# Optimization experiments

Measured on AMD Instinct MI355X. Metric: run time of the kernel, lower is better.

## Reference

```python
import jax, jax.numpy as jnp
import numpy as np
from math import sqrt

MIN_WINDOW, MAX_WINDOW = 1.0, 10000.0


def rope_consecutive(x):
    # x: [B, S, H, D]; TE 'consecutive' rotary: pairs are adjacent (even, odd) lanes.
    d = x.shape[-1]
    half = d // 2
    fraction = 2.0 * jnp.arange(half, dtype=jnp.float32) / d
    time_scales = MIN_WINDOW * (MAX_WINDOW / MIN_WINDOW) ** fraction          # [D/2]
    time_scales = jnp.repeat(time_scales, 2)                                   # [D]
    positions = jnp.arange(x.shape[1], dtype=jnp.float32)                      # [S]
    sinusoid = positions[None, :, None, None] / time_scales                    # [1,S,1,D]
    sin, cos = jnp.sin(sinusoid), jnp.cos(sinusoid)
    idx = jnp.arange(d)
    odd = (idx % 2) == 1                                                       # [D]
    # even lanes take left neighbor (roll -1), odd lanes take right neighbor (roll +1)
    x_shifted = jnp.where(odd, jnp.roll(x, 1, axis=-1), jnp.roll(x, -1, axis=-1))
    sign = jnp.where(odd, 1.0, -1.0)
    return (x * cos + x_shifted * sin * sign).astype(x.dtype)


def setup_inputs() -> dict:
    key = jax.random.key(0)
    k1, k2, k3 = jax.random.split(key, 3)
    B, S, M, H, D = 4, 2048, 2048, 16, 128
    x = jax.random.normal(k1, (B, S, M), dtype=jnp.float32)
    Wqkv = jax.random.normal(k2, (M, 3, H, D), dtype=jnp.float32) / sqrt(M)
    Wo = jax.random.normal(k3, (H * D, M), dtype=jnp.float32) / sqrt(H * D)
    return {"x": x, "Wqkv": Wqkv, "Wo": Wo}


def reference(x, Wqkv, Wo):
    # x: [B,S,M]; Wqkv: [M,3,H,D]; Wo: [H*D,M]
    B, S, M = x.shape
    H, D = Wqkv.shape[2], Wqkv.shape[3]
    qkv = jnp.einsum('bsm,mthd->bsthd', x, Wqkv)  # packed BS3HD projection
    q, k, v = qkv[:, :, 0], qkv[:, :, 1], qkv[:, :, 2]  # each [B,S,H,D]
    q = rope_consecutive(q)
    k = rope_consecutive(k)
    scale = 1.0 / sqrt(D)
    scores = jnp.einsum('bqhd,bkhd->bhqk', q, k) * scale  # [B,H,S,S]
    causal = jnp.tril(jnp.ones((S, S), dtype=bool))
    scores = jnp.where(causal[None, None], scores, jnp.finfo(scores.dtype).min)
    probs = jax.nn.softmax(scores, axis=-1)
    ctx = jnp.einsum('bhqk,bkhd->bqhd', probs, v)  # [B,S,H,D]
    out = jnp.einsum('bqhd,xm->bqm', ctx, jnp.zeros((0, 0))) if False else ctx.reshape(B, S, H * D) @ Wo
    return out
```

## Files before the change

kernel.cpp:

```cpp
#include <hip/hip_runtime.h>
#include <hip/hip_bf16.h>

#define B_ 4
#define S_ 2048
#define M_ 2048
#define H_ 16
#define D_ 128
#define ROWS (B_*S_)
#define CQKV (3*H_*D_)

typedef __bf16 bf16x8 __attribute__((ext_vector_type(8)));
typedef float f32x4 __attribute__((ext_vector_type(4)));
typedef unsigned short u16x8 __attribute__((ext_vector_type(8)));
typedef unsigned short u16x4 __attribute__((ext_vector_type(4)));

__device__ __forceinline__ unsigned short f2bf(float x) {
    unsigned u = __builtin_bit_cast(unsigned, x);
    u += 0x7fffu + ((u >> 16) & 1u);
    return (unsigned short)(u >> 16);
}
__device__ __forceinline__ float bf2f(unsigned short u) {
    return __builtin_bit_cast(float, (unsigned)u << 16);
}

__device__ __forceinline__ void gld_lds16(const unsigned short* g, unsigned short* l) {
    __builtin_amdgcn_global_load_lds(
        (__attribute__((address_space(1))) void*)g,
        (__attribute__((address_space(3))) void*)l,
        16, 0, 0);
}


__global__ __launch_bounds__(256) void cvt_bf16(const float* __restrict__ in,
                                                unsigned short* __restrict__ out) {
    int idx = (blockIdx.x * 256 + threadIdx.x) * 4;
    float4 v = *(const float4*)&in[idx];
    u16x4 o = { f2bf(v.x), f2bf(v.y), f2bf(v.z), f2bf(v.w) };
    *(u16x4*)&out[idx] = o;
}

__global__ __launch_bounds__(256) void cvt_transpose(const float* __restrict__ in,
                                                     unsigned short* __restrict__ out,
                                                     int R, int C) {
    __shared__ unsigned short tile[32][33];
    int c0 = blockIdx.x * 32, r0 = blockIdx.y * 32;
    int tx = threadIdx.x, ty = threadIdx.y;
#pragma unroll
    for (int i = 0; i < 4; ++i)
        tile[ty + i * 8][tx] = f2bf(in[(size_t)(r0 + ty + i * 8) * C + c0 + tx]);
    __syncthreads();
#pragma unroll
    for (int i = 0; i < 4; ++i)
        out[(size_t)(c0 + ty + i * 8) * R + r0 + tx] = tile[tx][ty + i * 8];
}

__global__ __launch_bounds__(256) void vtrans(const unsigned short* __restrict__ in,
                                              unsigned short* __restrict__ out) {
    __shared__ unsigned short tile[32][33];
    int bh = blockIdx.z;
    int d0 = blockIdx.x * 32, s0 = blockIdx.y * 32;
    const unsigned short* ib = in + (size_t)bh * S_ * D_;
    unsigned short* ob = out + (size_t)bh * S_ * D_;
    int tx = threadIdx.x, ty = threadIdx.y;
#pragma unroll
    for (int i = 0; i < 4; ++i)
        tile[ty + i * 8][tx] = ib[(size_t)(s0 + ty + i * 8) * D_ + d0 + tx];
    __syncthreads();
#pragma unroll
    for (int i = 0; i < 4; ++i)
        ob[(size_t)(d0 + ty + i * 8) * S_ + s0 + tx] = tile[tx][ty + i * 8];
}


#define BM2 256
#define BN2 256
#define BK2 64
#define NT2 (M_/BK2)

#define STAGE(p_, u_, mat_, h_) do {                                                     \
        const unsigned short* _s = (mat_) ? Bg : Ag;                                     \
        const size_t _r = (size_t)((((mat_) ? c0 : r0) + (h_) * 128) + w * 8 + srow) * M_ \
                          + (u_) * BK2 + scol;                                           \
        unsigned short* _l = &lds[(p_) * 32768 + (mat_) * 16384 + (h_) * 8192 + w * 512]; \
        gld_lds16(&_s[_r], _l);                                                          \
        gld_lds16(&_s[_r + (size_t)64 * M_], _l + 4096);                                 \
    } while (0)

#define BAR() asm volatile("s_barrier" ::: "memory")

#define GEMM_MAIN_LOOP()                                                                  \
    const int srow = lane >> 3;                                                           \
    const int scol = ((lane & 7) ^ srow) * 8;                                             \
    const int axor = lcol & 7;                                                            \
    const int k0off = (lq ^ axor) * 8;                                                    \
    const int k1off = ((4 | lq) ^ axor) * 8;                                              \
    const int arow = wr * 8192 + lcol * 64;                                               \
    const int brow = 16384 + (wc >> 1) * 8192 + ((wc & 1) * 64 + lcol) * 64;              \
    f32x4 acc[8][4];                                                                      \
    _Pragma("unroll") for (int i = 0; i < 8; ++i)                                         \
        _Pragma("unroll") for (int j = 0; j < 4; ++j) acc[i][j] = (f32x4){0.f,0.f,0.f,0.f};\
    STAGE(0, 0, 0, 0); STAGE(0, 0, 0, 1); STAGE(0, 0, 1, 0); STAGE(0, 0, 1, 1);           \
    STAGE(1, 1, 1, 0); STAGE(1, 1, 1, 1);                                                 \
    asm volatile("s_waitcnt vmcnt(4)" ::: "memory");                                      \
    BAR();                                                                                \
    bf16x8 a[4][2], b[4][2];                                                              \
    for (int t = 0; t < NT2; ++t) {                                                       \
        const int bo = (t & 1) * 32768;                                                   \
        const int pn = (t + 1) & 1;                                                       \
        const int u1 = (t + 1 < NT2) ? (t + 1) : (NT2 - 1);                               \
        const int u2 = (t + 2 < NT2) ? (t + 2) : (NT2 - 1);                               \
        _Pragma("unroll") for (int i = 0; i < 4; ++i) {                                   \
            a[i][0] = *(const bf16x8*)&lds[bo + arow + i * 1024 + k0off];                  \
            a[i][1] = *(const bf16x8*)&lds[bo + arow + i * 1024 + k1off];                  \
        }                                                                                 \
        _Pragma("unroll") for (int j = 0; j < 2; ++j) {                                   \
            b[j][0] = *(const bf16x8*)&lds[bo + brow + j * 1024 + k0off];                  \
            b[j][1] = *(const bf16x8*)&lds[bo + brow + j * 1024 + k1off];                  \
        }                                                                                 \
        STAGE(pn, u1, 0, 0);                                                              \
        BAR();                                                                            \
        __builtin_amdgcn_s_setprio(1);                                                    \
        _Pragma("unroll") for (int i = 0; i < 4; ++i)                                     \
            _Pragma("unroll") for (int j = 0; j < 2; ++j) {                               \
                acc[i][j] = __builtin_amdgcn_mfma_f32_16x16x32_bf16(a[i][0], b[j][0], acc[i][j], 0, 0, 0); \
                acc[i][j] = __builtin_amdgcn_mfma_f32_16x16x32_bf16(a[i][1], b[j][1], acc[i][j], 0, 0, 0); \
            }                                                                             \
        __builtin_amdgcn_s_setprio(0);                                                    \
        BAR();                                                                            \
        _Pragma("unroll") for (int j = 2; j < 4; ++j) {                                   \
            b[j][0] = *(const bf16x8*)&lds[bo + brow + j * 1024 + k0off];                  \
            b[j][1] = *(const bf16x8*)&lds[bo + brow + j * 1024 + k1off];                  \
        }                                                                                 \
        STAGE(pn, u1, 0, 1);                                                              \
        BAR();                                                                            \
        __builtin_amdgcn_s_setprio(1);                                                    \
        _Pragma("unroll") for (int i = 0; i < 4; ++i)                                     \
            _Pragma("unroll") for (int j = 2; j < 4; ++j) {                               \
                acc[i][j] = __builtin_amdgcn_mfma_f32_16x16x32_bf16(a[i][0], b[j][0], acc[i][j], 0, 0, 0); \
                acc[i][j] = __builtin_amdgcn_mfma_f32_16x16x32_bf16(a[i][1], b[j][1], acc[i][j], 0, 0, 0); \
            }                                                                             \
        __builtin_amdgcn_s_setprio(0);                                                    \
        BAR();                                                                            \
        _Pragma("unroll") for (int i = 0; i < 4; ++i) {                                   \
            a[i][0] = *(const bf16x8*)&lds[bo + arow + (i + 4) * 1024 + k0off];            \
            a[i][1] = *(const bf16x8*)&lds[bo + arow + (i + 4) * 1024 + k1off];            \
        }                                                                                 \
        STAGE(t & 1, u2, 1, 0);                                                           \
        BAR();                                                                            \
        __builtin_amdgcn_s_setprio(1);                                                    \
        _Pragma("unroll") for (int i = 0; i < 4; ++i)                                     \
            _Pragma("unroll") for (int j = 2; j < 4; ++j) {                               \
                acc[i + 4][j] = __builtin_amdgcn_mfma_f32_16x16x32_bf16(a[i][0], b[j][0], acc[i + 4][j], 0, 0, 0); \
                acc[i + 4][j] = __builtin_amdgcn_mfma_f32_16x16x32_bf16(a[i][1], b[j][1], acc[i + 4][j], 0, 0, 0); \
            }                                                                             \
        __builtin_amdgcn_s_setprio(0);                                                    \
        BAR();                                                                            \
        STAGE(t & 1, u2, 1, 1);                                                           \
        BAR();                                                                            \
        __builtin_amdgcn_s_setprio(1);                                                    \
        _Pragma("unroll") for (int i = 0; i < 4; ++i)                                     \
            _Pragma("unroll") for (int j = 0; j < 2; ++j) {                               \
                acc[i + 4][j] = __builtin_amdgcn_mfma_f32_16x16x32_bf16(a[i][0], b[j][0], acc[i + 4][j], 0, 0, 0); \
                acc[i + 4][j] = __builtin_amdgcn_mfma_f32_16x16x32_bf16(a[i][1], b[j][1], acc[i + 4][j], 0, 0, 0); \
            }                                                                             \
        __builtin_amdgcn_s_setprio(0);                                                    \
        asm volatile("s_waitcnt vmcnt(4)" ::: "memory");                                  \
        BAR();                                                                            \
    }


__global__ __launch_bounds__(512, 2) void gemm_qkv_rope(
    const unsigned short* __restrict__ xb,
    const unsigned short* __restrict__ wT,
    unsigned short* __restrict__ qg,
    unsigned short* __restrict__ kg,
    unsigned short* __restrict__ vg) {
    __shared__ unsigned short lds[65536];

    const int tid = threadIdx.x;
    const int lane = tid & 63;
    const int w = tid >> 6;
    const int wr = w >> 2;
    const int wc = w & 3;
    const int lcol = lane & 15;
    const int lq = lane >> 4;

    const int lin = (int)(blockIdx.y * gridDim.x + blockIdx.x);
    const int swz = (lin & 7) * 96 + (lin >> 3);
    const int r0 = (swz / 24) * BM2;
    const int c0 = (swz % 24) * BN2;

    const unsigned short* Ag = xb;
    const unsigned short* Bg = wT;

    GEMM_MAIN_LOOP()

    asm volatile("s_waitcnt vmcnt(0)" ::: "memory");
    __syncthreads();

    const int tix = c0 >> 11;
    const bool do_rope = (tix < 2);
#pragma unroll
    for (int j = 0; j < 4; ++j) {
        const int lcolT = wc * 64 + j * 16 + lcol;
        const int d = lcolT & 127;
        float inv_ts = 0.f, sw = 0.f, cw = 1.f;
        if (do_rope) {
            inv_ts = exp2f(-(float)(d >> 1) * (13.28771237954945f / 64.0f));
            __sincosf(inv_ts, &sw, &cw);
        }
#pragma unroll
        for (int i = 0; i < 8; ++i) {
            const int rbase = wr * 128 + i * 16 + lq * 4;
            float sn = 0.f, cs = 1.f;
            if (do_rope) {
                int s0 = (r0 + rbase) & 2047;
                __sincosf((float)s0 * inv_ts, &sn, &cs);
            }
#pragma unroll
            for (int r = 0; r < 4; ++r) {
                const int rowT = rbase + r;
                float val = acc[i][j][r];
                float pr = __shfl_xor(val, 1);
                float v2 = val;
                if (do_rope) {
                    v2 = (d & 1) ? (val * cs + pr * sn) : (val * cs - pr * sn);
                    float ns = sn * cw + cs * sw;
                    float nc = cs * cw - sn * sw;
                    sn = ns; cs = nc;
                }
                const int ch = lcolT >> 3;
                const int cph = (ch & ~7) | ((ch ^ rowT) & 7);
                lds[rowT * 256 + cph * 8 + (lcolT & 7)] = f2bf(v2);
            }
        }
    }
    __syncthreads();

    const int hh = (c0 & 2047) >> 7;
    unsigned short* dst = (tix == 0) ? qg : (tix == 1) ? kg : vg;
    const int li = tid & 15;
    const int g = tid >> 4;
#pragma unroll
    for (int gi = 0; gi < 16; ++gi) {
        const int rh = g + gi * 32;
        const int row = rh >> 1, half = rh & 1;
        const int clog = half * 16 + li;
        const int cph = (clog & ~7) | ((clog ^ row) & 7);
        u16x8 v = *(const u16x8*)&lds[row * 256 + cph * 8];
        const int gr = r0 + row;
        const int s = gr & 2047, bb = gr >> 11;
        *(u16x8*)&dst[(size_t)((bb * H_ + hh + half) * S_ + s) * D_ + li * 8] = v;
    }
}


__global__ __launch_bounds__(512, 2) void gemm_out(
    const unsigned short* __restrict__ ctx,
    const unsigned short* __restrict__ woT,
    float* __restrict__ out) {
    __shared__ unsigned short lds[65536];

    const int tid = threadIdx.x;
    const int lane = tid & 63;
    const int w = tid >> 6;
    const int wr = w >> 2;
    const int wc = w & 3;
    const int lcol = lane & 15;
    const int lq = lane >> 4;

    const int lin = (int)(blockIdx.y * gridDim.x + blockIdx.x);
    const int swz = (lin & 7) * 32 + (lin >> 3);
    const int r0 = (swz >> 3) * BM2;
    const int c0 = (swz & 7) * BN2;

    const unsigned short* Ag = ctx;
    const unsigned short* Bg = woT;

    GEMM_MAIN_LOOP()

#pragma unroll
    for (int i = 0; i < 8; ++i) {
#pragma unroll
        for (int r = 0; r < 4; ++r) {
            int row = r0 + wr * 128 + i * 16 + lq * 4 + r;
#pragma unroll
            for (int j = 0; j < 4; ++j) {
                int col = c0 + wc * 64 + j * 16 + lcol;
                out[(size_t)row * M_ + col] = acc[i][j][r];
            }
        }
    }
}

#undef STAGE
#undef BAR


__global__ __launch_bounds__(256, 2) void attn(
    const unsigned short* __restrict__ qg,
    const unsigned short* __restrict__ kg,
    const unsigned short* __restrict__ vt,
    unsigned short* __restrict__ ctx) {
    __shared__ unsigned short Ks[64 * 136];
    __shared__ unsigned short VTs[128 * 72];
    __shared__ unsigned short Ps[128 * 72];

    const int tid = threadIdx.x, lane = tid & 63, wave = tid >> 6;

    const int lin = (int)(blockIdx.y * gridDim.x + blockIdx.x);
    const int idx = lin >> 3;
    const int bh = ((lin & 7) << 3) + (idx >> 4);
    const int q0 = (15 - (idx & 15)) * 128;
    const int q0w = q0 + wave * 32;
    const unsigned short* qb = qg + (size_t)bh * S_ * D_;
    const unsigned short* kb = kg + (size_t)bh * S_ * D_;
    const unsigned short* vtb = vt + (size_t)bh * S_ * D_;

    const int lcol = lane & 15;
    const int lq = lane >> 4;

    const float scale = 0.08838834764831845f;
    bf16x8 qf[2][4];
#pragma unroll
    for (int f = 0; f < 2; ++f)
#pragma unroll
        for (int kk = 0; kk < 4; ++kk) {
            u16x8 raw = *(const u16x8*)&qb[(size_t)(q0w + f * 16 + lcol) * D_ + kk * 32 + lq * 8];
            u16x8 sc8;
#pragma unroll
            for (int j = 0; j < 8; ++j) sc8[j] = f2bf(bf2f(raw[j]) * scale);
            qf[f][kk] = __builtin_bit_cast(bf16x8, sc8);
        }

    f32x4 o[2][8];
#pragma unroll
    for (int f = 0; f < 2; ++f)
#pragma unroll
        for (int ot = 0; ot < 8; ++ot) o[f][ot] = (f32x4){0.f, 0.f, 0.f, 0.f};
    float lsum[2][4] = {{0.f, 0.f, 0.f, 0.f}, {0.f, 0.f, 0.f, 0.f}};

    const int kv_last = q0 + 64;

    u16x8 kpre[4], vpre[4];
#pragma unroll
    for (int j = 0; j < 4; ++j) {
        int c = tid + j * 256;
        kpre[j] = *(const u16x8*)&kb[(size_t)(c >> 4) * D_ + (c & 15) * 8];
        vpre[j] = *(const u16x8*)&vtb[(size_t)(c >> 3) * S_ + (c & 7) * 8];
    }

    for (int kv0 = 0; kv0 <= kv_last; kv0 += 64) {
        __syncthreads();
#pragma unroll
        for (int j = 0; j < 4; ++j) {
            int c = tid + j * 256;
            *(u16x8*)&Ks[(c >> 4) * 136 + (c & 15) * 8] = kpre[j];
            *(u16x8*)&VTs[(c >> 3) * 72 + (c & 7) * 8] = vpre[j];
        }
        __syncthreads();
        if (kv0 + 64 <= kv_last) {
#pragma unroll
            for (int j = 0; j < 4; ++j) {
                int c = tid + j * 256;
                kpre[j] = *(const u16x8*)&kb[(size_t)(kv0 + 64 + (c >> 4)) * D_ + (c & 15) * 8];
                vpre[j] = *(const u16x8*)&vtb[(size_t)(c >> 3) * S_ + kv0 + 64 + (c & 7) * 8];
            }
        }

        if (kv0 <= q0w + 31) {
            f32x4 sc[2][4];
            __builtin_amdgcn_s_setprio(1);
#pragma unroll
            for (int nt = 0; nt < 4; ++nt) {
                f32x4 a0 = (f32x4){0.f, 0.f, 0.f, 0.f};
                f32x4 a1 = (f32x4){0.f, 0.f, 0.f, 0.f};
#pragma unroll
                for (int kk = 0; kk < 4; ++kk) {
                    bf16x8 kf = *(const bf16x8*)&Ks[(nt * 16 + lcol) * 136 + kk * 32 + lq * 8];
                    a0 = __builtin_amdgcn_mfma_f32_16x16x32_bf16(qf[0][kk], kf, a0, 0, 0, 0);
                    a1 = __builtin_amdgcn_mfma_f32_16x16x32_bf16(qf[1][kk], kf, a1, 0, 0, 0);
                }
                sc[0][nt] = a0; sc[1][nt] = a1;
            }
            __builtin_amdgcn_s_setprio(0);

#pragma unroll
            for (int f = 0; f < 2; ++f) {
                if (kv0 + 63 > q0w + f * 16) {
#pragma unroll
                    for (int nt = 0; nt < 4; ++nt)
#pragma unroll
                        for (int r = 0; r < 4; ++r) {
                            int skv = kv0 + nt * 16 + lcol;
                            int sq = q0w + f * 16 + lq * 4 + r;
                            float p = (skv > sq) ? 0.f : __expf(sc[f][nt][r]);
                            sc[f][nt][r] = p;
                            lsum[f][r] += p;
                        }
                } else {
#pragma unroll
                    for (int nt = 0; nt < 4; ++nt)
#pragma unroll
                        for (int r = 0; r < 4; ++r) {
                            float p = __expf(sc[f][nt][r]);
                            sc[f][nt][r] = p;
                            lsum[f][r] += p;
                        }
                }
#pragma unroll
                for (int nt = 0; nt < 4; ++nt)
#pragma unroll
                    for (int r = 0; r < 4; ++r)
                        Ps[(wave * 32 + f * 16 + lq * 4 + r) * 72 + nt * 16 + lcol] = f2bf(sc[f][nt][r]);
            }

            __builtin_amdgcn_s_setprio(1);
#pragma unroll
            for (int kk = 0; kk < 2; ++kk) {
                bf16x8 pf0 = *(const bf16x8*)&Ps[(wave * 32 + lcol) * 72 + kk * 32 + lq * 8];
                bf16x8 pf1 = *(const bf16x8*)&Ps[(wave * 32 + 16 + lcol) * 72 + kk * 32 + lq * 8];
#pragma unroll
                for (int ot = 0; ot < 8; ++ot) {
                    bf16x8 vf = *(const bf16x8*)&VTs[(ot * 16 + lcol) * 72 + kk * 32 + lq * 8];
                    o[0][ot] = __builtin_amdgcn_mfma_f32_16x16x32_bf16(pf0, vf, o[0][ot], 0, 0, 0);
                    o[1][ot] = __builtin_amdgcn_mfma_f32_16x16x32_bf16(pf1, vf, o[1][ot], 0, 0, 0);
                }
            }
            __builtin_amdgcn_s_setprio(0);
        }
    }

#pragma unroll
    for (int f = 0; f < 2; ++f)
#pragma unroll
        for (int r = 0; r < 4; ++r) {
#pragma unroll
            for (int off = 1; off < 16; off <<= 1) lsum[f][r] += __shfl_xor(lsum[f][r], off);
        }

    const int b = bh >> 4, h = bh & 15;
#pragma unroll
    for (int f = 0; f < 2; ++f)
#pragma unroll
        for (int r = 0; r < 4; ++r) {
            float invl = 1.0f / lsum[f][r];
            int s = q0w + f * 16 + lq * 4 + r;
#pragma unroll
            for (int ot = 0; ot < 8; ++ot) {
                int d = ot * 16 + lcol;
                ctx[(size_t)(b * S_ + s) * (H_ * D_) + h * D_ + d] = f2bf(o[f][ot][r] * invl);
            }
        }
}


extern "C" void kernel_launch(void* const* d_in, const int* in_sizes, int n_in,
                              void* d_out, int out_size, void* d_ws, size_t ws_size,
                              hipStream_t stream) {
    const float* x = (const float*)d_in[0];
    const float* Wqkv = (const float*)d_in[1];
    const float* Wo = (const float*)d_in[2];
    float* out = (float*)d_out;

    unsigned short* xb = (unsigned short*)d_ws;
    unsigned short* wT = xb + (size_t)ROWS * M_;
    unsigned short* woT = wT + (size_t)CQKV * M_;
    unsigned short* qg = woT + (size_t)M_ * M_;
    unsigned short* kg = qg + (size_t)B_ * H_ * S_ * D_;
    unsigned short* vg = kg + (size_t)B_ * H_ * S_ * D_;
    unsigned short* vtw = vg + (size_t)B_ * H_ * S_ * D_;
    unsigned short* ctxp = vtw + (size_t)B_ * H_ * S_ * D_;

    cvt_bf16<<<(ROWS * M_) / 1024, 256, 0, stream>>>(x, xb);
    cvt_transpose<<<dim3(CQKV / 32, M_ / 32), dim3(32, 8), 0, stream>>>(Wqkv, wT, M_, CQKV);
    cvt_transpose<<<dim3(M_ / 32, M_ / 32), dim3(32, 8), 0, stream>>>(Wo, woT, M_, M_);

    gemm_qkv_rope<<<dim3(CQKV / BN2, ROWS / BM2), 512, 0, stream>>>(xb, wT, qg, kg, vg);
    vtrans<<<dim3(D_ / 32, S_ / 32, B_ * H_), dim3(32, 8), 0, stream>>>(vg, vtw);
    attn<<<dim3(S_ / 128, B_ * H_), 256, 0, stream>>>(qg, kg, vtw, ctxp);
    gemm_out<<<dim3(M_ / BN2, ROWS / BM2), 512, 0, stream>>>(ctxp, woT, out);
}
```

Baseline: 579.4 us.

## Double-buffer attention K/V tiles, enlarge blocks, write QKV epilogue directly

The attention kernel now uses 512-thread blocks covering 256 query rows, with double-buffered K and V^T shared-memory tiles. This cuts the per-iteration barrier count and lets the next tile's stores overlap the current compute. The QKV GEMM epilogue drops the shared-memory staging and writes bf16 values straight to global memory with scalar 2-byte stores. That saves LDS traffic and two barriers but gives up coalesced 16-byte stores. The larger attention blocks also mean fewer blocks and coarser causal load balancing.

```diff
diff --git a/kernel.cpp b/kernel.cpp
--- a/kernel.cpp
+++ b/kernel.cpp
@@ -195,62 +195,50 @@
 
     GEMM_MAIN_LOOP()
 
-    asm volatile("s_waitcnt vmcnt(0)" ::: "memory");
-    __syncthreads();
-
-    const int tix = c0 >> 11;
-    const bool do_rope = (tix < 2);
-#pragma unroll
-    for (int j = 0; j < 4; ++j) {
-        const int lcolT = wc * 64 + j * 16 + lcol;
-        const int d = lcolT & 127;
-        float inv_ts = 0.f, sw = 0.f, cw = 1.f;
-        if (do_rope) {
-            inv_ts = exp2f(-(float)(d >> 1) * (13.28771237954945f / 64.0f));
+    const int colbase = c0 + wc * 64;
+    const int tix = colbase >> 11;
+    const int hh = (colbase & 2047) >> 7;
+    unsigned short* dst = (tix == 0) ? qg : (tix == 1) ? kg : vg;
+    if (tix < 2) {
+#pragma unroll
+        for (int j = 0; j < 4; ++j) {
+            const int d = (wc & 1) * 64 + j * 16 + lcol;
+            float inv_ts = exp2f(-(float)(d >> 1) * (13.28771237954945f / 64.0f));
+            float sw, cw;
             __sincosf(inv_ts, &sw, &cw);
-        }
-#pragma unroll
-        for (int i = 0; i < 8; ++i) {
-            const int rbase = wr * 128 + i * 16 + lq * 4;
-            float sn = 0.f, cs = 1.f;
-            if (do_rope) {
-                int s0 = (r0 + rbase) & 2047;
+#pragma unroll
+            for (int i = 0; i < 8; ++i) {
+                int row0 = r0 + wr * 128 + i * 16 + lq * 4;
+                int bb = row0 >> 11, s0 = row0 & 2047;
+                float sn, cs;
                 __sincosf((float)s0 * inv_ts, &sn, &cs);
-            }
-#pragma unroll
-            for (int r = 0; r < 4; ++r) {
-                const int rowT = rbase + r;
-                float val = acc[i][j][r];
-                float pr = __shfl_xor(val, 1);
-                float v2 = val;
-                if (do_rope) {
-                    v2 = (d & 1) ? (val * cs + pr * sn) : (val * cs - pr * sn);
+                size_t base = (size_t)((bb * H_ + hh) * S_ + s0) * D_ + d;
+#pragma unroll
+                for (int r = 0; r < 4; ++r) {
+                    float val = acc[i][j][r];
+                    float pr = __shfl_xor(val, 1);
+                    float v2 = (d & 1) ? (val * cs + pr * sn) : (val * cs - pr * sn);
+                    dst[base + (size_t)r * D_] = f2bf(v2);
                     float ns = sn * cw + cs * sw;
                     float nc = cs * cw - sn * sw;
                     sn = ns; cs = nc;
                 }
-                const int ch = lcolT >> 3;
-                const int cph = (ch & ~7) | ((ch ^ rowT) & 7);
-                lds[rowT * 256 + cph * 8 + (lcolT & 7)] = f2bf(v2);
-            }
-        }
-    }
-    __syncthreads();
-
-    const int hh = (c0 & 2047) >> 7;
-    unsigned short* dst = (tix == 0) ? qg : (tix == 1) ? kg : vg;
-    const int li = tid & 15;
-    const int g = tid >> 4;
-#pragma unroll
-    for (int gi = 0; gi < 16; ++gi) {
-        const int rh = g + gi * 32;
-        const int row = rh >> 1, half = rh & 1;
-        const int clog = half * 16 + li;
-        const int cph = (clog & ~7) | ((clog ^ row) & 7);
-        u16x8 v = *(const u16x8*)&lds[row * 256 + cph * 8];
-        const int gr = r0 + row;
-        const int s = gr & 2047, bb = gr >> 11;
-        *(u16x8*)&dst[(size_t)((bb * H_ + hh + half) * S_ + s) * D_ + li * 8] = v;
+            }
+        }
+    } else {
+#pragma unroll
+        for (int j = 0; j < 4; ++j) {
+            const int d = (wc & 1) * 64 + j * 16 + lcol;
+#pragma unroll
+            for (int i = 0; i < 8; ++i) {
+                int row0 = r0 + wr * 128 + i * 16 + lq * 4;
+                int bb = row0 >> 11, s0 = row0 & 2047;
+                size_t base = (size_t)((bb * H_ + hh) * S_ + s0) * D_ + d;
+#pragma unroll
+                for (int r = 0; r < 4; ++r)
+                    dst[base + (size_t)r * D_] = f2bf(acc[i][j][r]);
+            }
+        }
     }
 }
 
@@ -297,21 +285,21 @@
 #undef BAR
 
 
-__global__ __launch_bounds__(256, 2) void attn(
+__global__ __launch_bounds__(512, 2) void attn(
     const unsigned short* __restrict__ qg,
     const unsigned short* __restrict__ kg,
     const unsigned short* __restrict__ vt,
     unsigned short* __restrict__ ctx) {
-    __shared__ unsigned short Ks[64 * 136];
-    __shared__ unsigned short VTs[128 * 72];
-    __shared__ unsigned short Ps[128 * 72];
+    __shared__ unsigned short Ks[2][64 * 136];
+    __shared__ unsigned short VTs[2][128 * 72];
+    __shared__ unsigned short Ps[256 * 72];
 
     const int tid = threadIdx.x, lane = tid & 63, wave = tid >> 6;
 
-    const int lin = (int)(blockIdx.y * gridDim.x + blockIdx.x);
+    const int lin = (int)blockIdx.x;
     const int idx = lin >> 3;
-    const int bh = ((lin & 7) << 3) + (idx >> 4);
-    const int q0 = (15 - (idx & 15)) * 128;
+    const int bh = ((lin & 7) << 3) + (idx >> 3);
+    const int q0 = (7 - (idx & 7)) * 256;
     const int q0w = q0 + wave * 32;
     const unsigned short* qb = qg + (size_t)bh * S_ * D_;
     const unsigned short* kb = kg + (size_t)bh * S_ * D_;
@@ -340,29 +328,31 @@
         for (int ot = 0; ot < 8; ++ot) o[f][ot] = (f32x4){0.f, 0.f, 0.f, 0.f};
     float lsum[2][4] = {{0.f, 0.f, 0.f, 0.f}, {0.f, 0.f, 0.f, 0.f}};
 
-    const int kv_last = q0 + 64;
-
-    u16x8 kpre[4], vpre[4];
-#pragma unroll
-    for (int j = 0; j < 4; ++j) {
-        int c = tid + j * 256;
+    const int kv_last = q0 + 192;
+
+    u16x8 kpre[2], vpre[2];
+#pragma unroll
+    for (int j = 0; j < 2; ++j) {
+        int c = tid + j * 512;
         kpre[j] = *(const u16x8*)&kb[(size_t)(c >> 4) * D_ + (c & 15) * 8];
         vpre[j] = *(const u16x8*)&vtb[(size_t)(c >> 3) * S_ + (c & 7) * 8];
     }
+#pragma unroll
+    for (int j = 0; j < 2; ++j) {
+        int c = tid + j * 512;
+        *(u16x8*)&Ks[0][(c >> 4) * 136 + (c & 15) * 8] = kpre[j];
+        *(u16x8*)&VTs[0][(c >> 3) * 72 + (c & 7) * 8] = vpre[j];
+    }
+    __syncthreads();
 
     for (int kv0 = 0; kv0 <= kv_last; kv0 += 64) {
-        __syncthreads();
-#pragma unroll
-        for (int j = 0; j < 4; ++j) {
-            int c = tid + j * 256;
-            *(u16x8*)&Ks[(c >> 4) * 136 + (c & 15) * 8] = kpre[j];
-            *(u16x8*)&VTs[(c >> 3) * 72 + (c & 7) * 8] = vpre[j];
-        }
-        __syncthreads();
-        if (kv0 + 64 <= kv_last) {
-#pragma unroll
-            for (int j = 0; j < 4; ++j) {
-                int c = tid + j * 256;
+        const int cur = (kv0 >> 6) & 1;
+        const bool more = (kv0 + 64 <= kv_last);
+
+        if (more) {
+#pragma unroll
+            for (int j = 0; j < 2; ++j) {
+                int c = tid + j * 512;
                 kpre[j] = *(const u16x8*)&kb[(size_t)(kv0 + 64 + (c >> 4)) * D_ + (c & 15) * 8];
                 vpre[j] = *(const u16x8*)&vtb[(size_t)(c >> 3) * S_ + kv0 + 64 + (c & 7) * 8];
             }
@@ -377,7 +367,7 @@
                 f32x4 a1 = (f32x4){0.f, 0.f, 0.f, 0.f};
 #pragma unroll
                 for (int kk = 0; kk < 4; ++kk) {
-                    bf16x8 kf = *(const bf16x8*)&Ks[(nt * 16 + lcol) * 136 + kk * 32 + lq * 8];
+                    bf16x8 kf = *(const bf16x8*)&Ks[cur][(nt * 16 + lcol) * 136 + kk * 32 + lq * 8];
                     a0 = __builtin_amdgcn_mfma_f32_16x16x32_bf16(qf[0][kk], kf, a0, 0, 0, 0);
                     a1 = __builtin_amdgcn_mfma_f32_16x16x32_bf16(qf[1][kk], kf, a1, 0, 0, 0);
                 }
@@ -422,13 +412,23 @@
                 bf16x8 pf1 = *(const bf16x8*)&Ps[(wave * 32 + 16 + lcol) * 72 + kk * 32 + lq * 8];
 #pragma unroll
                 for (int ot = 0; ot < 8; ++ot) {
-                    bf16x8 vf = *(const bf16x8*)&VTs[(ot * 16 + lcol) * 72 + kk * 32 + lq * 8];
+                    bf16x8 vf = *(const bf16x8*)&VTs[cur][(ot * 16 + lcol) * 72 + kk * 32 + lq * 8];
                     o[0][ot] = __builtin_amdgcn_mfma_f32_16x16x32_bf16(pf0, vf, o[0][ot], 0, 0, 0);
                     o[1][ot] = __builtin_amdgcn_mfma_f32_16x16x32_bf16(pf1, vf, o[1][ot], 0, 0, 0);
                 }
             }
             __builtin_amdgcn_s_setprio(0);
         }
+
+        if (more) {
+#pragma unroll
+            for (int j = 0; j < 2; ++j) {
+                int c = tid + j * 512;
+                *(u16x8*)&Ks[cur ^ 1][(c >> 4) * 136 + (c & 15) * 8] = kpre[j];
+                *(u16x8*)&VTs[cur ^ 1][(c >> 3) * 72 + (c & 7) * 8] = vpre[j];
+            }
+        }
+        __syncthreads();
     }
 
 #pragma unroll
@@ -478,6 +478,6 @@
 
     gemm_qkv_rope<<<dim3(CQKV / BN2, ROWS / BM2), 512, 0, stream>>>(xb, wT, qg, kg, vg);
     vtrans<<<dim3(D_ / 32, S_ / 32, B_ * H_), dim3(32, 8), 0, stream>>>(vg, vtw);
-    attn<<<dim3(S_ / 128, B_ * H_), 256, 0, stream>>>(qg, kg, vtw, ctxp);
+    attn<<<dim3((S_ / 256) * (B_ * H_)), 512, 0, stream>>>(qg, kg, vtw, ctxp);
     gemm_out<<<dim3(M_ / BN2, ROWS / BM2), 512, 0, stream>>>(ctxp, woT, out);
 }
```

Result: no change. 590.6 us (+1.9%).

## Fuse V transpose into QKV GEMM epilogue and write outputs directly from registers

Applied to the files above, without the earlier changes.

Removes the separate vtrans kernel by having the QKV GEMM epilogue write V already transposed ([B,H,D,S]) as 4-element vectors along S. It also drops the LDS staging in the epilogue and scatters Q/K results straight from accumulators to global memory. This saves a kernel launch, one full round trip of V through HBM, and two barriers. In exchange, Q/K stores become 2-byte scattered writes with poor coalescing instead of 16-byte row-contiguous stores.

```diff
diff --git a/kernel.cpp b/kernel.cpp
--- a/kernel.cpp
+++ b/kernel.cpp
@@ -52,23 +52,6 @@
 #pragma unroll
     for (int i = 0; i < 4; ++i)
         out[(size_t)(c0 + ty + i * 8) * R + r0 + tx] = tile[tx][ty + i * 8];
-}
-
-__global__ __launch_bounds__(256) void vtrans(const unsigned short* __restrict__ in,
-                                              unsigned short* __restrict__ out) {
-    __shared__ unsigned short tile[32][33];
-    int bh = blockIdx.z;
-    int d0 = blockIdx.x * 32, s0 = blockIdx.y * 32;
-    const unsigned short* ib = in + (size_t)bh * S_ * D_;
-    unsigned short* ob = out + (size_t)bh * S_ * D_;
-    int tx = threadIdx.x, ty = threadIdx.y;
-#pragma unroll
-    for (int i = 0; i < 4; ++i)
-        tile[ty + i * 8][tx] = ib[(size_t)(s0 + ty + i * 8) * D_ + d0 + tx];
-    __syncthreads();
-#pragma unroll
-    for (int i = 0; i < 4; ++i)
-        ob[(size_t)(d0 + ty + i * 8) * S_ + s0 + tx] = tile[tx][ty + i * 8];
 }
 
 
@@ -174,7 +157,7 @@
     const unsigned short* __restrict__ wT,
     unsigned short* __restrict__ qg,
     unsigned short* __restrict__ kg,
-    unsigned short* __restrict__ vg) {
+    unsigned short* __restrict__ vt) {
     __shared__ unsigned short lds[65536];
 
     const int tid = threadIdx.x;
@@ -195,62 +178,49 @@
 
     GEMM_MAIN_LOOP()
 
-    asm volatile("s_waitcnt vmcnt(0)" ::: "memory");
-    __syncthreads();
-
-    const int tix = c0 >> 11;
-    const bool do_rope = (tix < 2);
-#pragma unroll
-    for (int j = 0; j < 4; ++j) {
-        const int lcolT = wc * 64 + j * 16 + lcol;
-        const int d = lcolT & 127;
-        float inv_ts = 0.f, sw = 0.f, cw = 1.f;
-        if (do_rope) {
-            inv_ts = exp2f(-(float)(d >> 1) * (13.28771237954945f / 64.0f));
+    const int colbase = c0 + wc * 64;
+    const int tix = colbase >> 11;
+    const int hh = (colbase & 2047) >> 7;
+    if (tix < 2) {
+        unsigned short* dst = (tix == 0) ? qg : kg;
+#pragma unroll
+        for (int j = 0; j < 4; ++j) {
+            const int d = (wc & 1) * 64 + j * 16 + lcol;
+            float inv_ts = exp2f(-(float)(d >> 1) * (13.28771237954945f / 64.0f));
+            float sw, cw;
             __sincosf(inv_ts, &sw, &cw);
-        }
-#pragma unroll
-        for (int i = 0; i < 8; ++i) {
-            const int rbase = wr * 128 + i * 16 + lq * 4;
-            float sn = 0.f, cs = 1.f;
-            if (do_rope) {
-                int s0 = (r0 + rbase) & 2047;
+#pragma unroll
+            for (int i = 0; i < 8; ++i) {
+                int row0 = r0 + wr * 128 + i * 16 + lq * 4;
+                int bb = row0 >> 11, s0 = row0 & 2047;
+                float sn, cs;
                 __sincosf((float)s0 * inv_ts, &sn, &cs);
-            }
-#pragma unroll
-            for (int r = 0; r < 4; ++r) {
-                const int rowT = rbase + r;
-                float val = acc[i][j][r];
-                float pr = __shfl_xor(val, 1);
-                float v2 = val;
-                if (do_rope) {
-                    v2 = (d & 1) ? (val * cs + pr * sn) : (val * cs - pr * sn);
+                size_t base = (size_t)((bb * H_ + hh) * S_ + s0) * D_ + d;
+#pragma unroll
+                for (int r = 0; r < 4; ++r) {
+                    float val = acc[i][j][r];
+                    float pr = __shfl_xor(val, 1);
+                    float v2 = (d & 1) ? (val * cs + pr * sn) : (val * cs - pr * sn);
+                    dst[base + (size_t)r * D_] = f2bf(v2);
                     float ns = sn * cw + cs * sw;
                     float nc = cs * cw - sn * sw;
                     sn = ns; cs = nc;
                 }
-                const int ch = lcolT >> 3;
-                const int cph = (ch & ~7) | ((ch ^ rowT) & 7);
-                lds[rowT * 256 + cph * 8 + (lcolT & 7)] = f2bf(v2);
-            }
-        }
-    }
-    __syncthreads();
-
-    const int hh = (c0 & 2047) >> 7;
-    unsigned short* dst = (tix == 0) ? qg : (tix == 1) ? kg : vg;
-    const int li = tid & 15;
-    const int g = tid >> 4;
-#pragma unroll
-    for (int gi = 0; gi < 16; ++gi) {
-        const int rh = g + gi * 32;
-        const int row = rh >> 1, half = rh & 1;
-        const int clog = half * 16 + li;
-        const int cph = (clog & ~7) | ((clog ^ row) & 7);
-        u16x8 v = *(const u16x8*)&lds[row * 256 + cph * 8];
-        const int gr = r0 + row;
-        const int s = gr & 2047, bb = gr >> 11;
-        *(u16x8*)&dst[(size_t)((bb * H_ + hh + half) * S_ + s) * D_ + li * 8] = v;
+            }
+        }
+    } else {
+#pragma unroll
+        for (int j = 0; j < 4; ++j) {
+            const int d = (wc & 1) * 64 + j * 16 + lcol;
+#pragma unroll
+            for (int i = 0; i < 8; ++i) {
+                int row0 = r0 + wr * 128 + i * 16 + lq * 4;
+                int bb = row0 >> 11, s0 = row0 & 2047;
+                u16x4 v4 = { f2bf(acc[i][j][0]), f2bf(acc[i][j][1]),
+                             f2bf(acc[i][j][2]), f2bf(acc[i][j][3]) };
+                *(u16x4*)&vt[(size_t)((bb * H_ + hh) * D_ + d) * S_ + s0] = v4;
+            }
+        }
     }
 }
 
@@ -468,16 +438,14 @@
     unsigned short* woT = wT + (size_t)CQKV * M_;
     unsigned short* qg = woT + (size_t)M_ * M_;
     unsigned short* kg = qg + (size_t)B_ * H_ * S_ * D_;
-    unsigned short* vg = kg + (size_t)B_ * H_ * S_ * D_;
-    unsigned short* vtw = vg + (size_t)B_ * H_ * S_ * D_;
+    unsigned short* vtw = kg + (size_t)B_ * H_ * S_ * D_;
     unsigned short* ctxp = vtw + (size_t)B_ * H_ * S_ * D_;
 
     cvt_bf16<<<(ROWS * M_) / 1024, 256, 0, stream>>>(x, xb);
     cvt_transpose<<<dim3(CQKV / 32, M_ / 32), dim3(32, 8), 0, stream>>>(Wqkv, wT, M_, CQKV);
     cvt_transpose<<<dim3(M_ / 32, M_ / 32), dim3(32, 8), 0, stream>>>(Wo, woT, M_, M_);
 
-    gemm_qkv_rope<<<dim3(CQKV / BN2, ROWS / BM2), 512, 0, stream>>>(xb, wT, qg, kg, vg);
-    vtrans<<<dim3(D_ / 32, S_ / 32, B_ * H_), dim3(32, 8), 0, stream>>>(vg, vtw);
+    gemm_qkv_rope<<<dim3(CQKV / BN2, ROWS / BM2), 512, 0, stream>>>(xb, wT, qg, kg, vtw);
     attn<<<dim3(S_ / 128, B_ * H_), 256, 0, stream>>>(qg, kg, vtw, ctxp);
     gemm_out<<<dim3(M_ / BN2, ROWS / BM2), 512, 0, stream>>>(ctxp, woT, out);
 }
```

New measurement: 566.1 us. -2.3%, faster.
